# Kernel optimization log

Measured on AMD Instinct MI355X. Metric: run time of the kernel, lower is better.

## Reference

```python
import jax, jax.numpy as jnp
import numpy as np

BS, N, D, R = 16, 512, 256, 2


def setup_inputs() -> dict:
    key = jax.random.key(0)
    ks = jax.random.split(key, 9)
    s = 1.0 / np.sqrt(D)
    return {
        "encoded_spans": jax.random.normal(ks[0], (BS, N, D), dtype=jnp.float32),
        "w_rel1": jax.random.normal(ks[1], (R, D, D), dtype=jnp.float32) * s,
        "w_root1": jax.random.normal(ks[2], (D, D), dtype=jnp.float32) * s,
        "b1": jnp.zeros((D,), dtype=jnp.float32),
        "w_rel2": jax.random.normal(ks[3], (R, D, D), dtype=jnp.float32) * s,
        "w_root2": jax.random.normal(ks[4], (D, D), dtype=jnp.float32) * s,
        "b2": jnp.zeros((D,), dtype=jnp.float32),
        "aug_adj": jax.random.randint(ks[5], (BS, N, N), 0, 16, dtype=jnp.int64),
        "punct_graph": jax.random.randint(ks[6], (BS, N, N), 0, 16, dtype=jnp.int64),
    }


def reference(encoded_spans, w_rel1, w_root1, b1, w_rel2, w_root2, b2,
              aug_adj, punct_graph):
    # Edge-type masks, exactly as in the torch forward:
    #   type 0: punct edges not in aug graph; type 1: aug edges.
    mask_punct = (punct_graph == 1) & (aug_adj != 1)
    mask_aug = aug_adj == 1
    # masks[r, b, i, j] == 1 means an edge whose message flows x[b,i] -> node j
    # (edge_index = [b*N+i, b*N+j]; PyG aggregates x[src] into edge_index[1]).
    masks = jnp.stack([mask_punct, mask_aug]).astype(encoded_spans.dtype)  # [R,BS,N,N]
    # Per-relation in-degree of each target node (PyG RGCNConv aggr='mean';
    # empty neighborhoods aggregate to 0, i.e. divide by max(deg,1)).
    deg = jnp.maximum(masks.sum(axis=2), 1.0)[..., None]  # [R,BS,N,1]

    def conv(x, w_rel, w_root, b):
        # root/self transform + bias
        out = jnp.einsum('bnd,de->bne', x, w_root) + b
        for r in range(R):
            # mean-aggregate source features into targets, then relation weight
            agg = jnp.einsum('bij,bid->bjd', masks[r], x) / deg[r]
            out = out + jnp.einsum('bjd,de->bje', agg, w_rel[r])
        return out

    # dropout is identity in eval mode
    h = jax.nn.elu(conv(encoded_spans, w_rel1, w_root1, b1))
    h = jax.nn.elu(conv(h, w_rel2, w_root2, b2))
    return h
```

## Files before the change

### kernel.cpp

```cpp
#include <hip/hip_runtime.h>
#include <hip/hip_bf16.h>

#define BS 16
#define NN 512
#define DD 256
#define RR 2
#define M_TOT (BS * NN)
#define KCAT 768

typedef __attribute__((ext_vector_type(8))) short short8;
typedef __attribute__((ext_vector_type(4))) float f32x4;

static __device__ __forceinline__ ushort f2bf(float f) {
  __hip_bfloat16 h = __float2bfloat16(f);
  return *reinterpret_cast<ushort*>(&h);
}

__global__ __launch_bounds__(256) void masks_kernel(
    const int* __restrict__ aug, const int* __restrict__ punct,
    unsigned long long* __restrict__ bitsT) {
  int j = blockIdx.x * 256 + threadIdx.x;
  int w = blockIdx.y;
  int b = blockIdx.z;
  long base = ((long)(b * NN + w * 64)) * NN + j;
  unsigned long long m0 = 0ull, m1 = 0ull;
#pragma unroll 16
  for (int k = 0; k < 64; ++k) {
    int a = aug[base + (long)k * NN];
    int p = punct[base + (long)k * NN];
    unsigned long long isa = (unsigned long long)(a == 1);
    unsigned long long isp = (unsigned long long)((p == 1) & (a != 1));
    m1 |= isa << k;
    m0 |= isp << k;
  }
  bitsT[((0 * BS + b) * NN + j) * 8 + w] = m0;
  bitsT[((1 * BS + b) * NN + j) * 8 + w] = m1;
}

__global__ __launch_bounds__(256) void mt_kernel(
    const unsigned long long* __restrict__ bitsT, ushort* __restrict__ MT,
    float* __restrict__ inv_deg) {
  int j = blockIdx.x, b = blockIdx.y;
  __shared__ unsigned long long words[2][8];
  int t = threadIdx.x;
  if (t < 16)
    words[t >> 3][t & 7] = bitsT[((t >> 3) * BS + b) * NN * 8 + j * 8 + (t & 7)];
  __syncthreads();
  if (t < 2) {
    int s = 0;
#pragma unroll
    for (int w = 0; w < 8; ++w) s += __popcll(words[t][w]);
    if (s < 1) s = 1;
    inv_deg[(t * BS + b) * NN + j] = 1.0f / (float)s;
  }
  int i0 = t * 2;
  int w = i0 >> 6;
#pragma unroll
  for (int r = 0; r < 2; ++r) {
    unsigned long long v = words[r][w] >> (i0 & 63);
    unsigned int packed = ((v & 1) ? 0x3F80u : 0u) | ((v & 2) ? 0x3F800000u : 0u);
    unsigned int* row = reinterpret_cast<unsigned int*>(
        MT + ((size_t)((r * BS + b) * NN + j)) * NN);
    row[t] = packed;
  }
}

__global__ void xprep_kernel(const float* __restrict__ x,
                             ushort* __restrict__ Abig1,
                             ushort* __restrict__ xT) {
  __shared__ float tile[32][33];
  int i0 = blockIdx.x * 32, d0 = blockIdx.y * 32, b = blockIdx.z;
  int tx = threadIdx.x, ty = threadIdx.y;
#pragma unroll
  for (int q = 0; q < 4; ++q) {
    int il = ty + q * 8;
    tile[il][tx] = x[((long)(b * NN + i0 + il)) * DD + d0 + tx];
  }
  __syncthreads();
#pragma unroll
  for (int q = 0; q < 4; ++q) {
    int il = ty + q * 8;
    Abig1[(size_t)(b * NN + i0 + il) * KCAT + d0 + tx] = f2bf(tile[il][tx]);
  }
#pragma unroll
  for (int q = 0; q < 4; ++q) {
    int dl = ty + q * 8;
    xT[((size_t)(b * DD + d0 + dl)) * NN + i0 + tx] = f2bf(tile[tx][dl]);
  }
}

__global__ void transpose_h_kernel(const ushort* __restrict__ A2,
                                   ushort* __restrict__ hT) {
  __shared__ ushort tile[32][33];
  int i0 = blockIdx.x * 32, d0 = blockIdx.y * 32, b = blockIdx.z;
  int tx = threadIdx.x, ty = threadIdx.y;
#pragma unroll
  for (int q = 0; q < 4; ++q) {
    int il = ty + q * 8;
    tile[il][tx] = A2[((long)(b * NN + i0 + il)) * KCAT + d0 + tx];
  }
  __syncthreads();
#pragma unroll
  for (int q = 0; q < 4; ++q) {
    int dl = ty + q * 8;
    hT[((long)(b * DD + d0 + dl)) * NN + i0 + tx] = tile[tx][dl];
  }
}

__global__ void wcat_kernel(const float* __restrict__ wroot1,
                            const float* __restrict__ wrel1,
                            const float* __restrict__ wroot2,
                            const float* __restrict__ wrel2,
                            ushort* __restrict__ W1, ushort* __restrict__ W2) {
  __shared__ float tile[32][33];
  int z = blockIdx.z;
  int layer = z / 3, s = z % 3;
  const float* root = layer ? wroot2 : wroot1;
  const float* rel = layer ? wrel2 : wrel1;
  ushort* dst = layer ? W2 : W1;
  const float* src = (s == 0) ? root : (rel + (size_t)(s - 1) * DD * DD);
  int d0 = blockIdx.x * 32, e0 = blockIdx.y * 32;
  int tx = threadIdx.x, ty = threadIdx.y;
#pragma unroll
  for (int q = 0; q < 4; ++q) {
    int dl = ty + q * 8;
    tile[dl][tx] = src[((long)(d0 + dl)) * DD + e0 + tx];
  }
  __syncthreads();
#pragma unroll
  for (int q = 0; q < 4; ++q) {
    int el = ty + q * 8;
    dst[((size_t)(e0 + el)) * KCAT + s * 256 + d0 + tx] = f2bf(tile[tx][el]);
  }
}

__global__ __launch_bounds__(256) void agg_gemm_kernel(
    const ushort* __restrict__ MT, const ushort* __restrict__ xT,
    const float* __restrict__ inv_deg, ushort* __restrict__ Abig) {
  __shared__ __align__(16) ushort As[2][128][40];
  __shared__ __align__(16) ushort Bs[2][64][40];
  int t = threadIdx.x;
  int rb = blockIdx.z;
  int r = rb >> 4, b = rb & 15;
  int m_base = blockIdx.y * 128;
  int n_base = blockIdx.x * 64;
  int srow = t >> 2, scol = (t & 3) * 8;

  const ushort* Ag0 = MT + ((size_t)((r * BS + b) * NN + m_base + srow)) * NN + scol;
  const ushort* Ag1 = Ag0 + (size_t)64 * NN;
  const ushort* Bg = xT + ((size_t)(b * DD + n_base + srow)) * NN + scol;

  int wave = t >> 6, lane = t & 63;
  int wm = wave >> 1, wn = wave & 1;
  int fr = lane & 15, fq = lane >> 4;

  f32x4 acc[4][2];
#pragma unroll
  for (int i = 0; i < 4; ++i)
#pragma unroll
    for (int jj = 0; jj < 2; ++jj) acc[i][jj] = (f32x4)(0.0f);

  const int NT = NN / 32;
  int4 pa0A, pa1A, pbA, pa0B, pa1B, pbB;
  pa0A = *reinterpret_cast<const int4*>(Ag0);
  pa1A = *reinterpret_cast<const int4*>(Ag1);
  pbA  = *reinterpret_cast<const int4*>(Bg);
  pa0B = *reinterpret_cast<const int4*>(Ag0 + 32);
  pa1B = *reinterpret_cast<const int4*>(Ag1 + 32);
  pbB  = *reinterpret_cast<const int4*>(Bg + 32);
  *reinterpret_cast<int4*>(&As[0][srow][scol]) = pa0A;
  *reinterpret_cast<int4*>(&As[0][64 + srow][scol]) = pa1A;
  *reinterpret_cast<int4*>(&Bs[0][srow][scol]) = pbA;
  __syncthreads();

#pragma unroll 2
  for (int kt = 0; kt < NT; ++kt) {
    if (kt + 2 < NT) {
      pa0A = *reinterpret_cast<const int4*>(Ag0 + (kt + 2) * 32);
      pa1A = *reinterpret_cast<const int4*>(Ag1 + (kt + 2) * 32);
      pbA  = *reinterpret_cast<const int4*>(Bg + (kt + 2) * 32);
    }
    int cur = kt & 1;
    short8 a0 = *reinterpret_cast<const short8*>(&As[cur][wm * 64 + fr][fq * 8]);
    short8 a1 = *reinterpret_cast<const short8*>(&As[cur][wm * 64 + 16 + fr][fq * 8]);
    short8 a2 = *reinterpret_cast<const short8*>(&As[cur][wm * 64 + 32 + fr][fq * 8]);
    short8 a3 = *reinterpret_cast<const short8*>(&As[cur][wm * 64 + 48 + fr][fq * 8]);
    short8 b0 = *reinterpret_cast<const short8*>(&Bs[cur][wn * 32 + fr][fq * 8]);
    short8 b1 = *reinterpret_cast<const short8*>(&Bs[cur][wn * 32 + 16 + fr][fq * 8]);
    acc[0][0] = __builtin_amdgcn_mfma_f32_16x16x32_bf16(a0, b0, acc[0][0], 0, 0, 0);
    acc[0][1] = __builtin_amdgcn_mfma_f32_16x16x32_bf16(a0, b1, acc[0][1], 0, 0, 0);
    acc[1][0] = __builtin_amdgcn_mfma_f32_16x16x32_bf16(a1, b0, acc[1][0], 0, 0, 0);
    acc[1][1] = __builtin_amdgcn_mfma_f32_16x16x32_bf16(a1, b1, acc[1][1], 0, 0, 0);
    acc[2][0] = __builtin_amdgcn_mfma_f32_16x16x32_bf16(a2, b0, acc[2][0], 0, 0, 0);
    acc[2][1] = __builtin_amdgcn_mfma_f32_16x16x32_bf16(a2, b1, acc[2][1], 0, 0, 0);
    acc[3][0] = __builtin_amdgcn_mfma_f32_16x16x32_bf16(a3, b0, acc[3][0], 0, 0, 0);
    acc[3][1] = __builtin_amdgcn_mfma_f32_16x16x32_bf16(a3, b1, acc[3][1], 0, 0, 0);
    if (kt + 1 < NT) {
      int nxt = cur ^ 1;
      *reinterpret_cast<int4*>(&As[nxt][srow][scol]) = pa0B;
      *reinterpret_cast<int4*>(&As[nxt][64 + srow][scol]) = pa1B;
      *reinterpret_cast<int4*>(&Bs[nxt][srow][scol]) = pbB;
    }
    __syncthreads();
    pa0B = pa0A; pa1B = pa1A; pbB = pbA;
  }

  const float* idg = inv_deg + (r * BS + b) * NN + m_base;
#pragma unroll
  for (int mi = 0; mi < 4; ++mi) {
#pragma unroll
    for (int t4 = 0; t4 < 4; ++t4) {
      int jl = wm * 64 + mi * 16 + fq * 4 + t4;
      float idv = idg[jl];
      size_t rowoff =
          (size_t)(b * NN + m_base + jl) * KCAT + 256 + r * 256 + n_base;
#pragma unroll
      for (int ni = 0; ni < 2; ++ni) {
        int d = wn * 32 + ni * 16 + fr;
        Abig[rowoff + d] = f2bf(acc[mi][ni][t4] * idv);
      }
    }
  }
}

template <int MODE>
__global__ __launch_bounds__(256) void main_gemm_kernel(
    const ushort* __restrict__ A, const ushort* __restrict__ WcatT,
    const float* __restrict__ bias, ushort* __restrict__ hOut,
    float* __restrict__ fOut) {
  __shared__ __align__(16) ushort As[2][64][40];
  __shared__ __align__(16) ushort Bs[2][64][40];
  int t = threadIdx.x;
  int m_base = blockIdx.y * 64;
  int n_base = blockIdx.x * 64;
  int srow = t >> 2, scol = (t & 3) * 8;
  const ushort* Ag = A + (size_t)(m_base + srow) * KCAT + scol;
  const ushort* Bg = WcatT + (size_t)(n_base + srow) * KCAT + scol;

  int wave = t >> 6, lane = t & 63;
  int wm = wave >> 1, wn = wave & 1;
  int fr = lane & 15, fq = lane >> 4;

  f32x4 acc[2][2];
#pragma unroll
  for (int i = 0; i < 2; ++i)
#pragma unroll
    for (int jj = 0; jj < 2; ++jj) acc[i][jj] = (f32x4)(0.0f);

  const int NT = KCAT / 32;
  int4 paA, pbA, paB, pbB;
  paA = *reinterpret_cast<const int4*>(Ag);
  pbA = *reinterpret_cast<const int4*>(Bg);
  paB = *reinterpret_cast<const int4*>(Ag + 32);
  pbB = *reinterpret_cast<const int4*>(Bg + 32);
  *reinterpret_cast<int4*>(&As[0][srow][scol]) = paA;
  *reinterpret_cast<int4*>(&Bs[0][srow][scol]) = pbA;
  __syncthreads();

#pragma unroll 2
  for (int kt = 0; kt < NT; ++kt) {
    if (kt + 2 < NT) {
      paA = *reinterpret_cast<const int4*>(Ag + (kt + 2) * 32);
      pbA = *reinterpret_cast<const int4*>(Bg + (kt + 2) * 32);
    }
    int cur = kt & 1;
    short8 a0 = *reinterpret_cast<const short8*>(&As[cur][wm * 32 + fr][fq * 8]);
    short8 a1 = *reinterpret_cast<const short8*>(&As[cur][wm * 32 + 16 + fr][fq * 8]);
    short8 b0 = *reinterpret_cast<const short8*>(&Bs[cur][wn * 32 + fr][fq * 8]);
    short8 b1 = *reinterpret_cast<const short8*>(&Bs[cur][wn * 32 + 16 + fr][fq * 8]);
    acc[0][0] = __builtin_amdgcn_mfma_f32_16x16x32_bf16(a0, b0, acc[0][0], 0, 0, 0);
    acc[0][1] = __builtin_amdgcn_mfma_f32_16x16x32_bf16(a0, b1, acc[0][1], 0, 0, 0);
    acc[1][0] = __builtin_amdgcn_mfma_f32_16x16x32_bf16(a1, b0, acc[1][0], 0, 0, 0);
    acc[1][1] = __builtin_amdgcn_mfma_f32_16x16x32_bf16(a1, b1, acc[1][1], 0, 0, 0);
    if (kt + 1 < NT) {
      int nxt = cur ^ 1;
      *reinterpret_cast<int4*>(&As[nxt][srow][scol]) = paB;
      *reinterpret_cast<int4*>(&Bs[nxt][srow][scol]) = pbB;
    }
    __syncthreads();
    paB = paA; pbB = pbA;
  }

#pragma unroll
  for (int mi = 0; mi < 2; ++mi) {
#pragma unroll
    for (int t4 = 0; t4 < 4; ++t4) {
      int m = m_base + wm * 32 + mi * 16 + fq * 4 + t4;
#pragma unroll
      for (int ni = 0; ni < 2; ++ni) {
        int e = n_base + wn * 32 + ni * 16 + fr;
        float v = acc[mi][ni][t4] + bias[e];
        v = v > 0.0f ? v : expm1f(v);
        if (MODE == 0)
          hOut[(size_t)m * KCAT + e] = f2bf(v);
        else
          fOut[(size_t)m * DD + e] = v;
      }
    }
  }
}

extern "C" void kernel_launch(void* const* d_in, const int* in_sizes, int n_in,
                              void* d_out, int out_size, void* d_ws,
                              size_t ws_size, hipStream_t stream) {
  const float* x = (const float*)d_in[0];
  const float* w_rel1 = (const float*)d_in[1];
  const float* w_root1 = (const float*)d_in[2];
  const float* b1 = (const float*)d_in[3];
  const float* w_rel2 = (const float*)d_in[4];
  const float* w_root2 = (const float*)d_in[5];
  const float* b2 = (const float*)d_in[6];
  const int* aug = (const int*)d_in[7];
  const int* punct = (const int*)d_in[8];
  float* out = (float*)d_out;

  char* ws = (char*)d_ws;
  size_t off = 0;
  unsigned long long* bitsT = (unsigned long long*)(ws + off); off += (size_t)RR * BS * NN * 8 * 8;
  float* inv_deg = (float*)(ws + off);                         off += (size_t)RR * BS * NN * 4;
  ushort* MT = (ushort*)(ws + off);                            off += (size_t)RR * BS * NN * NN * 2;
  ushort* xT = (ushort*)(ws + off);                            off += (size_t)BS * DD * NN * 2;
  ushort* WcatT1 = (ushort*)(ws + off);                        off += (size_t)DD * KCAT * 2;
  ushort* WcatT2 = (ushort*)(ws + off);                        off += (size_t)DD * KCAT * 2;
  ushort* Abig1 = (ushort*)(ws + off);                         off += (size_t)M_TOT * KCAT * 2;
  ushort* Abig2 = (ushort*)(ws + off);                         off += (size_t)M_TOT * KCAT * 2;

  masks_kernel<<<dim3(2, 8, 16), 256, 0, stream>>>(aug, punct, bitsT);
  mt_kernel<<<dim3(NN, BS), 256, 0, stream>>>(bitsT, MT, inv_deg);

  xprep_kernel<<<dim3(16, 8, 16), dim3(32, 8), 0, stream>>>(x, Abig1, xT);
  wcat_kernel<<<dim3(8, 8, 6), dim3(32, 8), 0, stream>>>(w_root1, w_rel1,
                                                         w_root2, w_rel2,
                                                         WcatT1, WcatT2);

  agg_gemm_kernel<<<dim3(4, 4, 32), 256, 0, stream>>>(MT, xT, inv_deg, Abig1);
  main_gemm_kernel<0><<<dim3(4, 128), 256, 0, stream>>>(Abig1, WcatT1, b1,
                                                        Abig2, nullptr);

  transpose_h_kernel<<<dim3(16, 8, 16), dim3(32, 8), 0, stream>>>(Abig2, xT);
  agg_gemm_kernel<<<dim3(4, 4, 32), 256, 0, stream>>>(MT, xT, inv_deg, Abig2);
  main_gemm_kernel<1><<<dim3(4, 128), 256, 0, stream>>>(Abig2, WcatT2, b2,
                                                        nullptr, out);
}
```

Baseline: 179.3 us.

## Use direct global-to-LDS loads in GEMMs and fuse h transpose into epilogue

Replaces register-staged double buffering in both GEMM kernels with global_load_lds direct-to-LDS copies into unpadded 32-wide tiles. The layer-1 main GEMM epilogue now also writes a transposed copy of h through LDS into a separate hT buffer, which removes the standalone transpose kernel launch and its extra pass over the activation. Unpadded LDS rows may cause bank conflicts on the MFMA fragment reads. The loop prefetches only one tile ahead instead of two, which may expose more load latency.

```diff
diff --git a/kernel.cpp b/kernel.cpp
--- a/kernel.cpp
+++ b/kernel.cpp
@@ -10,6 +10,11 @@
 
 typedef __attribute__((ext_vector_type(8))) short short8;
 typedef __attribute__((ext_vector_type(4))) float f32x4;
+typedef const __attribute__((address_space(1))) unsigned int as1u32;
+typedef __attribute__((address_space(3))) unsigned int as3u32;
+
+#define GLDS16(g, l) \
+  __builtin_amdgcn_global_load_lds((as1u32*)(g), (as3u32*)(l), 16, 0, 0)
 
 static __device__ __forceinline__ ushort f2bf(float f) {
   __hip_bfloat16 h = __float2bfloat16(f);
@@ -89,24 +94,6 @@
   }
 }
 
-__global__ void transpose_h_kernel(const ushort* __restrict__ A2,
-                                   ushort* __restrict__ hT) {
-  __shared__ ushort tile[32][33];
-  int i0 = blockIdx.x * 32, d0 = blockIdx.y * 32, b = blockIdx.z;
-  int tx = threadIdx.x, ty = threadIdx.y;
-#pragma unroll
-  for (int q = 0; q < 4; ++q) {
-    int il = ty + q * 8;
-    tile[il][tx] = A2[((long)(b * NN + i0 + il)) * KCAT + d0 + tx];
-  }
-  __syncthreads();
-#pragma unroll
-  for (int q = 0; q < 4; ++q) {
-    int dl = ty + q * 8;
-    hT[((long)(b * DD + d0 + dl)) * NN + i0 + tx] = tile[tx][dl];
-  }
-}
-
 __global__ void wcat_kernel(const float* __restrict__ wroot1,
                             const float* __restrict__ wrel1,
                             const float* __restrict__ wroot2,
@@ -137,22 +124,18 @@
 __global__ __launch_bounds__(256) void agg_gemm_kernel(
     const ushort* __restrict__ MT, const ushort* __restrict__ xT,
     const float* __restrict__ inv_deg, ushort* __restrict__ Abig) {
-  __shared__ __align__(16) ushort As[2][128][40];
-  __shared__ __align__(16) ushort Bs[2][64][40];
+  __shared__ __align__(16) ushort As[2][128 * 32];
+  __shared__ __align__(16) ushort Bs[2][64 * 32];
   int t = threadIdx.x;
-  int rb = blockIdx.z;
-  int r = rb >> 4, b = rb & 15;
-  int m_base = blockIdx.y * 128;
-  int n_base = blockIdx.x * 64;
-  int srow = t >> 2, scol = (t & 3) * 8;
-
-  const ushort* Ag0 = MT + ((size_t)((r * BS + b) * NN + m_base + srow)) * NN + scol;
-  const ushort* Ag1 = Ag0 + (size_t)64 * NN;
-  const ushort* Bg = xT + ((size_t)(b * DD + n_base + srow)) * NN + scol;
-
-  int wave = t >> 6, lane = t & 63;
-  int wm = wave >> 1, wn = wave & 1;
-  int fr = lane & 15, fq = lane >> 4;
+  int wv = t >> 6, ln = t & 63;
+  int fr = ln & 15, fq = ln >> 4;
+  int rb = blockIdx.z, r = rb >> 4, b = rb & 15;
+  int m_base = blockIdx.y * 128, n_base = blockIdx.x * 64;
+
+  const ushort* Ag = MT + ((size_t)((r * BS + b) * NN + m_base)) * NN;
+  const ushort* Bg = xT + ((size_t)(b * DD + n_base)) * NN;
+  int srow = ln >> 2;
+  int scol = (ln & 3) * 8;
 
   f32x4 acc[4][2];
 #pragma unroll
@@ -160,49 +143,46 @@
 #pragma unroll
     for (int jj = 0; jj < 2; ++jj) acc[i][jj] = (f32x4)(0.0f);
 
+#pragma unroll
+  for (int q = 0; q < 2; ++q) {
+    int c = wv * 2 + q;
+    GLDS16(Ag + (size_t)(c * 16 + srow) * NN + scol, &As[0][c * 512]);
+  }
+  GLDS16(Bg + (size_t)(wv * 16 + srow) * NN + scol, &Bs[0][wv * 512]);
+  __syncthreads();
+
   const int NT = NN / 32;
-  int4 pa0A, pa1A, pbA, pa0B, pa1B, pbB;
-  pa0A = *reinterpret_cast<const int4*>(Ag0);
-  pa1A = *reinterpret_cast<const int4*>(Ag1);
-  pbA  = *reinterpret_cast<const int4*>(Bg);
-  pa0B = *reinterpret_cast<const int4*>(Ag0 + 32);
-  pa1B = *reinterpret_cast<const int4*>(Ag1 + 32);
-  pbB  = *reinterpret_cast<const int4*>(Bg + 32);
-  *reinterpret_cast<int4*>(&As[0][srow][scol]) = pa0A;
-  *reinterpret_cast<int4*>(&As[0][64 + srow][scol]) = pa1A;
-  *reinterpret_cast<int4*>(&Bs[0][srow][scol]) = pbA;
-  __syncthreads();
-
-#pragma unroll 2
+  int wm = wv >> 1, wn = wv & 1;
+#pragma unroll 1
   for (int kt = 0; kt < NT; ++kt) {
-    if (kt + 2 < NT) {
-      pa0A = *reinterpret_cast<const int4*>(Ag0 + (kt + 2) * 32);
-      pa1A = *reinterpret_cast<const int4*>(Ag1 + (kt + 2) * 32);
-      pbA  = *reinterpret_cast<const int4*>(Bg + (kt + 2) * 32);
+    int cur = kt & 1;
+    if (kt + 1 < NT) {
+      int k0 = (kt + 1) * 32;
+#pragma unroll
+      for (int q = 0; q < 2; ++q) {
+        int c = wv * 2 + q;
+        GLDS16(Ag + (size_t)(c * 16 + srow) * NN + k0 + scol,
+               &As[cur ^ 1][c * 512]);
+      }
+      GLDS16(Bg + (size_t)(wv * 16 + srow) * NN + k0 + scol,
+             &Bs[cur ^ 1][wv * 512]);
     }
-    int cur = kt & 1;
-    short8 a0 = *reinterpret_cast<const short8*>(&As[cur][wm * 64 + fr][fq * 8]);
-    short8 a1 = *reinterpret_cast<const short8*>(&As[cur][wm * 64 + 16 + fr][fq * 8]);
-    short8 a2 = *reinterpret_cast<const short8*>(&As[cur][wm * 64 + 32 + fr][fq * 8]);
-    short8 a3 = *reinterpret_cast<const short8*>(&As[cur][wm * 64 + 48 + fr][fq * 8]);
-    short8 b0 = *reinterpret_cast<const short8*>(&Bs[cur][wn * 32 + fr][fq * 8]);
-    short8 b1 = *reinterpret_cast<const short8*>(&Bs[cur][wn * 32 + 16 + fr][fq * 8]);
-    acc[0][0] = __builtin_amdgcn_mfma_f32_16x16x32_bf16(a0, b0, acc[0][0], 0, 0, 0);
-    acc[0][1] = __builtin_amdgcn_mfma_f32_16x16x32_bf16(a0, b1, acc[0][1], 0, 0, 0);
-    acc[1][0] = __builtin_amdgcn_mfma_f32_16x16x32_bf16(a1, b0, acc[1][0], 0, 0, 0);
-    acc[1][1] = __builtin_amdgcn_mfma_f32_16x16x32_bf16(a1, b1, acc[1][1], 0, 0, 0);
-    acc[2][0] = __builtin_amdgcn_mfma_f32_16x16x32_bf16(a2, b0, acc[2][0], 0, 0, 0);
-    acc[2][1] = __builtin_amdgcn_mfma_f32_16x16x32_bf16(a2, b1, acc[2][1], 0, 0, 0);
-    acc[3][0] = __builtin_amdgcn_mfma_f32_16x16x32_bf16(a3, b0, acc[3][0], 0, 0, 0);
-    acc[3][1] = __builtin_amdgcn_mfma_f32_16x16x32_bf16(a3, b1, acc[3][1], 0, 0, 0);
-    if (kt + 1 < NT) {
-      int nxt = cur ^ 1;
-      *reinterpret_cast<int4*>(&As[nxt][srow][scol]) = pa0B;
-      *reinterpret_cast<int4*>(&As[nxt][64 + srow][scol]) = pa1B;
-      *reinterpret_cast<int4*>(&Bs[nxt][srow][scol]) = pbB;
-    }
+    short8 a[4], bb[2];
+#pragma unroll
+    for (int mi = 0; mi < 4; ++mi)
+      a[mi] = *reinterpret_cast<const short8*>(
+          &As[cur][(wm * 64 + mi * 16 + fr) * 32 + fq * 8]);
+#pragma unroll
+    for (int ni = 0; ni < 2; ++ni)
+      bb[ni] = *reinterpret_cast<const short8*>(
+          &Bs[cur][(wn * 32 + ni * 16 + fr) * 32 + fq * 8]);
+#pragma unroll
+    for (int mi = 0; mi < 4; ++mi)
+#pragma unroll
+      for (int ni = 0; ni < 2; ++ni)
+        acc[mi][ni] = __builtin_amdgcn_mfma_f32_16x16x32_bf16(
+            a[mi], bb[ni], acc[mi][ni], 0, 0, 0);
     __syncthreads();
-    pa0B = pa0A; pa1B = pa1A; pbB = pbA;
   }
 
   const float* idg = inv_deg + (r * BS + b) * NN + m_base;
@@ -225,21 +205,20 @@
 
 template <int MODE>
 __global__ __launch_bounds__(256) void main_gemm_kernel(
-    const ushort* __restrict__ A, const ushort* __restrict__ WcatT,
+    const ushort* __restrict__ A, const ushort* __restrict__ WT,
     const float* __restrict__ bias, ushort* __restrict__ hOut,
-    float* __restrict__ fOut) {
-  __shared__ __align__(16) ushort As[2][64][40];
-  __shared__ __align__(16) ushort Bs[2][64][40];
+    ushort* __restrict__ hT, float* __restrict__ fOut) {
+  __shared__ __align__(16) ushort As[2][64 * 32];
+  __shared__ __align__(16) ushort Bs[2][64 * 32];
   int t = threadIdx.x;
-  int m_base = blockIdx.y * 64;
-  int n_base = blockIdx.x * 64;
-  int srow = t >> 2, scol = (t & 3) * 8;
-  const ushort* Ag = A + (size_t)(m_base + srow) * KCAT + scol;
-  const ushort* Bg = WcatT + (size_t)(n_base + srow) * KCAT + scol;
-
-  int wave = t >> 6, lane = t & 63;
-  int wm = wave >> 1, wn = wave & 1;
-  int fr = lane & 15, fq = lane >> 4;
+  int wv = t >> 6, ln = t & 63;
+  int fr = ln & 15, fq = ln >> 4;
+  int m_base = blockIdx.y * 64, e_base = blockIdx.x * 64;
+
+  const ushort* Ag = A + (size_t)m_base * KCAT;
+  const ushort* Bg = WT + (size_t)e_base * KCAT;
+  int srow = ln >> 2;
+  int scol = (ln & 3) * 8;
 
   f32x4 acc[2][2];
 #pragma unroll
@@ -247,56 +226,93 @@
 #pragma unroll
     for (int jj = 0; jj < 2; ++jj) acc[i][jj] = (f32x4)(0.0f);
 
+  GLDS16(Ag + (size_t)(wv * 16 + srow) * KCAT + scol, &As[0][wv * 512]);
+  GLDS16(Bg + (size_t)(wv * 16 + srow) * KCAT + scol, &Bs[0][wv * 512]);
+  __syncthreads();
+
   const int NT = KCAT / 32;
-  int4 paA, pbA, paB, pbB;
-  paA = *reinterpret_cast<const int4*>(Ag);
-  pbA = *reinterpret_cast<const int4*>(Bg);
-  paB = *reinterpret_cast<const int4*>(Ag + 32);
-  pbB = *reinterpret_cast<const int4*>(Bg + 32);
-  *reinterpret_cast<int4*>(&As[0][srow][scol]) = paA;
-  *reinterpret_cast<int4*>(&Bs[0][srow][scol]) = pbA;
-  __syncthreads();
-
-#pragma unroll 2
+  int wm = wv >> 1, wn = wv & 1;
+#pragma unroll 1
   for (int kt = 0; kt < NT; ++kt) {
-    if (kt + 2 < NT) {
-      paA = *reinterpret_cast<const int4*>(Ag + (kt + 2) * 32);
-      pbA = *reinterpret_cast<const int4*>(Bg + (kt + 2) * 32);
+    int cur = kt & 1;
+    if (kt + 1 < NT) {
+      int k0 = (kt + 1) * 32;
+      GLDS16(Ag + (size_t)(wv * 16 + srow) * KCAT + k0 + scol,
+             &As[cur ^ 1][wv * 512]);
+      GLDS16(Bg + (size_t)(wv * 16 + srow) * KCAT + k0 + scol,
+             &Bs[cur ^ 1][wv * 512]);
     }
-    int cur = kt & 1;
-    short8 a0 = *reinterpret_cast<const short8*>(&As[cur][wm * 32 + fr][fq * 8]);
-    short8 a1 = *reinterpret_cast<const short8*>(&As[cur][wm * 32 + 16 + fr][fq * 8]);
-    short8 b0 = *reinterpret_cast<const short8*>(&Bs[cur][wn * 32 + fr][fq * 8]);
-    short8 b1 = *reinterpret_cast<const short8*>(&Bs[cur][wn * 32 + 16 + fr][fq * 8]);
-    acc[0][0] = __builtin_amdgcn_mfma_f32_16x16x32_bf16(a0, b0, acc[0][0], 0, 0, 0);
-    acc[0][1] = __builtin_amdgcn_mfma_f32_16x16x32_bf16(a0, b1, acc[0][1], 0, 0, 0);
-    acc[1][0] = __builtin_amdgcn_mfma_f32_16x16x32_bf16(a1, b0, acc[1][0], 0, 0, 0);
-    acc[1][1] = __builtin_amdgcn_mfma_f32_16x16x32_bf16(a1, b1, acc[1][1], 0, 0, 0);
-    if (kt + 1 < NT) {
-      int nxt = cur ^ 1;
-      *reinterpret_cast<int4*>(&As[nxt][srow][scol]) = paB;
-      *reinterpret_cast<int4*>(&Bs[nxt][srow][scol]) = pbB;
-    }
+    short8 a[2], bb[2];
+#pragma unroll
+    for (int mi = 0; mi < 2; ++mi)
+      a[mi] = *reinterpret_cast<const short8*>(
+          &As[cur][(wm * 32 + mi * 16 + fr) * 32 + fq * 8]);
+#pragma unroll
+    for (int ni = 0; ni < 2; ++ni)
+      bb[ni] = *reinterpret_cast<const short8*>(
+          &Bs[cur][(wn * 32 + ni * 16 + fr) * 32 + fq * 8]);
+#pragma unroll
+    for (int mi = 0; mi < 2; ++mi)
+#pragma unroll
+      for (int ni = 0; ni < 2; ++ni)
+        acc[mi][ni] = __builtin_amdgcn_mfma_f32_16x16x32_bf16(
+            a[mi], bb[ni], acc[mi][ni], 0, 0, 0);
     __syncthreads();
-    paB = paA; pbB = pbA;
-  }
-
-#pragma unroll
-  for (int mi = 0; mi < 2; ++mi) {
-#pragma unroll
-    for (int t4 = 0; t4 < 4; ++t4) {
-      int m = m_base + wm * 32 + mi * 16 + fq * 4 + t4;
-#pragma unroll
-      for (int ni = 0; ni < 2; ++ni) {
-        int e = n_base + wn * 32 + ni * 16 + fr;
-        float v = acc[mi][ni][t4] + bias[e];
-        v = v > 0.0f ? v : expm1f(v);
-        if (MODE == 0)
-          hOut[(size_t)m * KCAT + e] = f2bf(v);
-        else
+  }
+
+  float bsv[2];
+#pragma unroll
+  for (int ni = 0; ni < 2; ++ni) bsv[ni] = bias[e_base + wn * 32 + ni * 16 + fr];
+
+  if (MODE == 1) {
+#pragma unroll
+    for (int mi = 0; mi < 2; ++mi)
+#pragma unroll
+      for (int t4 = 0; t4 < 4; ++t4) {
+        int m = m_base + wm * 32 + mi * 16 + fq * 4 + t4;
+#pragma unroll
+        for (int ni = 0; ni < 2; ++ni) {
+          int e = e_base + wn * 32 + ni * 16 + fr;
+          float v = acc[mi][ni][t4] + bsv[ni];
+          v = v > 0.0f ? v : expm1f(v);
           fOut[(size_t)m * DD + e] = v;
+        }
       }
-    }
+  } else {
+    int b = m_base >> 9, j0 = m_base & (NN - 1);
+    ushort* LT = &As[0][0];
+    ushort hv[2][2][4];
+#pragma unroll
+    for (int mi = 0; mi < 2; ++mi)
+#pragma unroll
+      for (int ni = 0; ni < 2; ++ni)
+#pragma unroll
+        for (int t4 = 0; t4 < 4; ++t4) {
+          int m = m_base + wm * 32 + mi * 16 + fq * 4 + t4;
+          int e = e_base + wn * 32 + ni * 16 + fr;
+          float v = acc[mi][ni][t4] + bsv[ni];
+          v = v > 0.0f ? v : expm1f(v);
+          ushort u = f2bf(v);
+          hOut[(size_t)m * KCAT + e] = u;
+          hv[mi][ni][t4] = u;
+        }
+#pragma unroll
+    for (int mi = 0; mi < 2; ++mi)
+#pragma unroll
+      for (int ni = 0; ni < 2; ++ni)
+#pragma unroll
+        for (int t4 = 0; t4 < 4; ++t4) {
+          int ml = wm * 32 + mi * 16 + fq * 4 + t4;
+          int el = wn * 32 + ni * 16 + fr;
+          LT[el * 68 + ml] = hv[mi][ni][t4];
+        }
+    __syncthreads();
+    int er = t >> 2, mq = (t & 3) * 16;
+    ushort* dst = hT + ((size_t)(b * DD + e_base + er)) * NN + j0 + mq;
+    int4 v0 = *reinterpret_cast<const int4*>(&LT[er * 68 + mq]);
+    int4 v1 = *reinterpret_cast<const int4*>(&LT[er * 68 + mq + 8]);
+    *reinterpret_cast<int4*>(dst) = v0;
+    *reinterpret_cast<int4*>(dst + 8) = v1;
   }
 }
 
@@ -320,6 +336,7 @@
   float* inv_deg = (float*)(ws + off);                         off += (size_t)RR * BS * NN * 4;
   ushort* MT = (ushort*)(ws + off);                            off += (size_t)RR * BS * NN * NN * 2;
   ushort* xT = (ushort*)(ws + off);                            off += (size_t)BS * DD * NN * 2;
+  ushort* hT = (ushort*)(ws + off);                            off += (size_t)BS * DD * NN * 2;
   ushort* WcatT1 = (ushort*)(ws + off);                        off += (size_t)DD * KCAT * 2;
   ushort* WcatT2 = (ushort*)(ws + off);                        off += (size_t)DD * KCAT * 2;
   ushort* Abig1 = (ushort*)(ws + off);                         off += (size_t)M_TOT * KCAT * 2;
@@ -327,7 +344,6 @@
 
   masks_kernel<<<dim3(2, 8, 16), 256, 0, stream>>>(aug, punct, bitsT);
   mt_kernel<<<dim3(NN, BS), 256, 0, stream>>>(bitsT, MT, inv_deg);
-
   xprep_kernel<<<dim3(16, 8, 16), dim3(32, 8), 0, stream>>>(x, Abig1, xT);
   wcat_kernel<<<dim3(8, 8, 6), dim3(32, 8), 0, stream>>>(w_root1, w_rel1,
                                                          w_root2, w_rel2,
@@ -335,10 +351,8 @@
 
   agg_gemm_kernel<<<dim3(4, 4, 32), 256, 0, stream>>>(MT, xT, inv_deg, Abig1);
   main_gemm_kernel<0><<<dim3(4, 128), 256, 0, stream>>>(Abig1, WcatT1, b1,
-                                                        Abig2, nullptr);
-
-  transpose_h_kernel<<<dim3(16, 8, 16), dim3(32, 8), 0, stream>>>(Abig2, xT);
-  agg_gemm_kernel<<<dim3(4, 4, 32), 256, 0, stream>>>(MT, xT, inv_deg, Abig2);
+                                                        Abig2, hT, nullptr);
+  agg_gemm_kernel<<<dim3(4, 4, 32), 256, 0, stream>>>(MT, hT, inv_deg, Abig2);
   main_gemm_kernel<1><<<dim3(4, 128), 256, 0, stream>>>(Abig2, WcatT2, b2,
-                                                        nullptr, out);
-}
+                                                        nullptr, nullptr, out);
+}
```

Result: faster. 169.1 us (-5.7%).
